# Kernel tuning notes

Hardware: AMD Instinct MI355X
Metric: run time of the kernel (lower is better)

The kernel has to match this reference:

```python
import jax, jax.numpy as jnp
import numpy as np

N_NODES = 100000
N_EDGES = 3200000
F_IN = 256
H = 256
L = 256
BN_EPS = 1e-5


def gcn_conv(x, src, dst, deg_inv_sqrt, W, b):
    # x: [N, Fin]; src/dst: [E+N] (self-loops appended); returns [N, Fout]
    h = x @ W  # dense transform first (Fout may be < Fin)
    norm = deg_inv_sqrt[src] * deg_inv_sqrt[dst]  # [E+N]
    msg = h[src] * norm[:, None]                  # gather
    out = jax.ops.segment_sum(msg, dst, num_segments=N_NODES)  # scatter-add
    return out + b


def batch_norm(x, gamma, beta):
    # BatchNorm1d in training mode: per-feature mean/var over the node dim
    mean = jnp.mean(x, axis=0)
    var = jnp.var(x, axis=0)
    return (x - mean) * jax.lax.rsqrt(var + BN_EPS) * gamma + beta


def setup_inputs() -> dict:
    key = jax.random.key(0)
    ks = jax.random.split(key, 8)
    x = jax.random.normal(ks[0], (N_NODES, F_IN), dtype=jnp.float32)
    edge_index = jax.random.randint(ks[1], (2, N_EDGES), 0, N_NODES, dtype=jnp.int64)
    # glorot-ish init for weights
    W1 = jax.random.normal(ks[2], (F_IN, H), dtype=jnp.float32) * (1.0 / np.sqrt(F_IN))
    b1 = jnp.zeros((H,), dtype=jnp.float32)
    W_mu = jax.random.normal(ks[3], (H, L), dtype=jnp.float32) * (1.0 / np.sqrt(H))
    b_mu = jnp.zeros((L,), dtype=jnp.float32)
    W_ls = jax.random.normal(ks[4], (H, L), dtype=jnp.float32) * (1.0 / np.sqrt(H))
    b_ls = jnp.zeros((L,), dtype=jnp.float32)
    gamma = jnp.ones((H,), dtype=jnp.float32)
    beta = jnp.zeros((H,), dtype=jnp.float32)
    return {"x": x, "edge_index": edge_index, "W1": W1, "b1": b1,
            "W_mu": W_mu, "b_mu": b_mu, "W_ls": W_ls, "b_ls": b_ls,
            "gamma": gamma, "beta": beta}


def reference(x, edge_index, W1, b1, W_mu, b_mu, W_ls, b_ls, gamma, beta):
    # Add self-loops once (shared across the three GCNConv layers)
    loop = jnp.arange(N_NODES, dtype=edge_index.dtype)
    src = jnp.concatenate([edge_index[0], loop])
    dst = jnp.concatenate([edge_index[1], loop])
    deg = jax.ops.segment_sum(jnp.ones_like(dst, dtype=jnp.float32), dst,
                              num_segments=N_NODES)
    deg_inv_sqrt = jnp.where(deg > 0, jax.lax.rsqrt(jnp.maximum(deg, 1.0)), 0.0)

    h = gcn_conv(x, src, dst, deg_inv_sqrt, W1, b1)
    h = jax.nn.relu(batch_norm(h, gamma, beta))
    mu = gcn_conv(h, src, dst, deg_inv_sqrt, W_mu, b_mu)
    logstd = gcn_conv(h, src, dst, deg_inv_sqrt, W_ls, b_ls)
    return (mu, logstd)
```

## Files before the change

### kernel.cpp

```cpp
#include <hip/hip_runtime.h>
#include <hip/hip_bf16.h>

#define FEAT 256
#define NPB 512
#define NPB_SHIFT 9
#define MAXBINS 256
#define CAP 20480
#define BIN_CHUNK 8192

typedef __attribute__((ext_vector_type(8))) short bf16x8;
typedef __attribute__((ext_vector_type(8))) ushort u16x8;
typedef __attribute__((ext_vector_type(4))) float f32x4;

__device__ __forceinline__ float bf2f(ushort h) {
    union { unsigned u; float f; } v; v.u = ((unsigned)h) << 16; return v.f;
}
__device__ __forceinline__ ushort f2bf(float f) {
    union { float f; unsigned u; } v; v.f = f;
    unsigned u = v.u;
    return (ushort)((u + 0x7FFFu + ((u >> 16) & 1u)) >> 16);
}


__global__ __launch_bounds__(256) void k_bin(const int* __restrict__ ei, int E, int N,
                                             int* __restrict__ bincur,
                                             int2* __restrict__ binbuf, int nbins) {
    __shared__ int hist[MAXBINS];
    __shared__ int base[MAXBINS];
    int t = threadIdx.x;
    int T = E + N;
    int start = blockIdx.x * BIN_CHUNK;
    int end = min(start + BIN_CHUNK, T);
    for (int b = t; b < nbins; b += 256) hist[b] = 0;
    __syncthreads();
    for (int idx = start + t; idx < end; idx += 256) {
        int d = (idx < E) ? ei[E + idx] : idx - E;
        atomicAdd(&hist[d >> NPB_SHIFT], 1);
    }
    __syncthreads();
    for (int b = t; b < nbins; b += 256) {
        int c = hist[b];
        base[b] = c ? (b * CAP + atomicAdd(&bincur[b], c)) : 0;
        hist[b] = 0;
    }
    __syncthreads();
    for (int idx = start + t; idx < end; idx += 256) {
        int s, d;
        if (idx < E) { s = ei[idx]; d = ei[E + idx]; }
        else         { s = idx - E; d = idx - E; }
        int b = d >> NPB_SHIFT;
        int local = atomicAdd(&hist[b], 1);
        binbuf[base[b] + local] = make_int2(s, d);
    }
}


__global__ __launch_bounds__(512) void k_scanb(const int* __restrict__ bsum,
                                               int* __restrict__ bpre,
                                               int* __restrict__ offs_n, int nb) {
    __shared__ int s[512];
    int t = threadIdx.x;
    int v = (t < nb) ? bsum[t] : 0;
    s[t] = v;
    __syncthreads();
    for (int d = 1; d < 512; d <<= 1) {
        int x = (t >= d) ? s[t - d] : 0;
        __syncthreads();
        s[t] += x;
        __syncthreads();
    }
    if (t < nb) bpre[t] = s[t] - v;
    if (t == nb - 1) offs_n[0] = s[t];
}


__global__ __launch_bounds__(512) void k_histcsr(const int2* __restrict__ binbuf,
                                                 const int* __restrict__ bincur,
                                                 const int* __restrict__ bpre,
                                                 int* __restrict__ offs,
                                                 float* __restrict__ dis,
                                                 int* __restrict__ csr, int N) {
    __shared__ int h[NPB];
    __shared__ int cur[NPB];
    int b = blockIdx.x;
    int t = threadIdx.x;
    int node0 = b * NPB;
    int nn = min(NPB, N - node0);
    h[t] = 0; cur[t] = 0;
    __syncthreads();
    int cnt = bincur[b];
    int base = b * CAP;
    for (int i = t; i < cnt; i += 512) {
        atomicAdd(&h[binbuf[base + i].y - node0], 1);
    }
    __syncthreads();
    int v = h[t];
    for (int d = 1; d < 512; d <<= 1) {
        int x = (t >= d) ? h[t - d] : 0;
        __syncthreads();
        h[t] += x;
        __syncthreads();
    }
    int myoff = bpre[b] + h[t] - v;
    if (t < nn) {
        offs[node0 + t] = myoff;
        dis[node0 + t] = rsqrtf((float)v);
    }
    h[t] = myoff;
    __syncthreads();
    for (int i = t; i < cnt; i += 512) {
        int2 e = binbuf[base + i];
        int ld = e.y - node0;
        int c = atomicAdd(&cur[ld], 1);
        csr[h[ld] + c] = e.x;
    }
}


__global__ __launch_bounds__(256) void k_cvt(const float* __restrict__ x,
                                             ushort* __restrict__ y,
                                             const float* __restrict__ dis, int n4) {
    int i = blockIdx.x * blockDim.x + threadIdx.x;
    int stride = gridDim.x * blockDim.x;
    for (; i < n4; i += stride) {
        float d = dis[i >> 6];
        float4 v = ((const float4*)x)[i];
        ushort4 o;
        o.x = f2bf(v.x * d); o.y = f2bf(v.y * d);
        o.z = f2bf(v.z * d); o.w = f2bf(v.w * d);
        ((ushort4*)y)[i] = o;
    }
}


__global__ void k_wprep(const float* __restrict__ W1, const float* __restrict__ Wmu,
                        const float* __restrict__ Wls, const float* __restrict__ bmu,
                        const float* __restrict__ bls,
                        ushort* __restrict__ Wt1, ushort* __restrict__ Wtc,
                        float* __restrict__ biasc, float* __restrict__ bnacc) {
    int i = blockIdx.x * 256 + threadIdx.x;
    int m = i >> 16;
    int j = i & 65535;
    int n = j >> 8, k = j & 255;
    const float* W = (m == 0) ? W1 : (m == 1) ? Wmu : Wls;
    ushort v = f2bf(W[k * 256 + n]);
    if (m == 0) Wt1[j] = v;
    else if (m == 1) Wtc[j] = v;
    else Wtc[65536 + j] = v;
    if (i < 512) { biasc[i] = (i < 256) ? bmu[i] : bls[i - 256]; bnacc[i] = 0.f; }
}


__global__ __launch_bounds__(256) void k_agg(const ushort* __restrict__ in,
                                             ushort* __restrict__ out,
                                             const int* __restrict__ offs,
                                             const int* __restrict__ csr,
                                             const float* __restrict__ dis, int N) {
    int wid = blockIdx.x * 4 + ((int)threadIdx.x >> 6);
    if (wid >= N) return;
    int lane = threadIdx.x & 63;
    int half = lane >> 5;
    int l32 = lane & 31;
    int beg = offs[wid], end = offs[wid + 1];
    float acc[8] = {};
    int k = beg;
    for (; k + 16 <= end; k += 16) {
        int s0 = csr[k + half];
        int s1 = csr[k + 2 + half];
        int s2 = csr[k + 4 + half];
        int s3 = csr[k + 6 + half];
        int s4 = csr[k + 8 + half];
        int s5 = csr[k + 10 + half];
        int s6 = csr[k + 12 + half];
        int s7 = csr[k + 14 + half];
        bf16x8 v0 = *(const bf16x8*)(in + (size_t)s0 * FEAT + l32 * 8);
        bf16x8 v1 = *(const bf16x8*)(in + (size_t)s1 * FEAT + l32 * 8);
        bf16x8 v2 = *(const bf16x8*)(in + (size_t)s2 * FEAT + l32 * 8);
        bf16x8 v3 = *(const bf16x8*)(in + (size_t)s3 * FEAT + l32 * 8);
        bf16x8 v4 = *(const bf16x8*)(in + (size_t)s4 * FEAT + l32 * 8);
        bf16x8 v5 = *(const bf16x8*)(in + (size_t)s5 * FEAT + l32 * 8);
        bf16x8 v6 = *(const bf16x8*)(in + (size_t)s6 * FEAT + l32 * 8);
        bf16x8 v7 = *(const bf16x8*)(in + (size_t)s7 * FEAT + l32 * 8);
        #pragma unroll
        for (int j = 0; j < 8; ++j) {
            float t0 = bf2f((ushort)v0[j]) + bf2f((ushort)v1[j]);
            float t1 = bf2f((ushort)v2[j]) + bf2f((ushort)v3[j]);
            float t2 = bf2f((ushort)v4[j]) + bf2f((ushort)v5[j]);
            float t3 = bf2f((ushort)v6[j]) + bf2f((ushort)v7[j]);
            acc[j] += (t0 + t1) + (t2 + t3);
        }
    }
    for (; k + 2 <= end; k += 2) {
        int s = csr[k + half];
        bf16x8 v = *(const bf16x8*)(in + (size_t)s * FEAT + l32 * 8);
        #pragma unroll
        for (int j = 0; j < 8; ++j) acc[j] += bf2f((ushort)v[j]);
    }
    if (k < end && half == 0) {
        int s = csr[k];
        bf16x8 v = *(const bf16x8*)(in + (size_t)s * FEAT + l32 * 8);
        #pragma unroll
        for (int j = 0; j < 8; ++j) acc[j] += bf2f((ushort)v[j]);
    }
    #pragma unroll
    for (int j = 0; j < 8; ++j) acc[j] += __shfl_xor(acc[j], 32, 64);
    if (half == 0) {
        float d = dis[wid];
        u16x8 o;
        #pragma unroll
        for (int j = 0; j < 8; ++j) o[j] = f2bf(acc[j] * d);
        *(u16x8*)(out + (size_t)wid * FEAT + l32 * 8) = o;
    }
}


template <bool BF16OUT>
__global__ __launch_bounds__(256) void k_gemm(const ushort* __restrict__ A,
                                              const ushort* __restrict__ Bt,
                                              const float* __restrict__ bias,
                                              float* __restrict__ C0,
                                              float* __restrict__ C1,
                                              ushort* __restrict__ Cb,
                                              float* __restrict__ bnacc,
                                              int M, int split) {
    __shared__ ushort As[128 * 64];
    __shared__ ushort Bs[128 * 64];
    int t = threadIdx.x;
    int lane = t & 63;
    int wave = t >> 6;
    int wrow = wave >> 1, wcol = wave & 1;
    int bx = blockIdx.x, by = blockIdx.y;
    int lo = lane & 15, g = lane >> 4;
    f32x4 acc[4][4] = {};
    int chunk = t & 7;
    int row4 = t >> 3;

    for (int kt = 0; kt < 4; ++kt) {
        int k0 = kt * 64;
        #pragma unroll
        for (int i = 0; i < 4; ++i) {
            int r = row4 + i * 32;
            int lc = chunk ^ (r & 7);
            int gr = by * 128 + r;
            bf16x8 av = {};
            if (gr < M) av = *(const bf16x8*)(A + (size_t)gr * 256 + k0 + lc * 8);
            *(bf16x8*)(As + r * 64 + chunk * 8) = av;
            int gn = bx * 128 + r;
            bf16x8 bv = *(const bf16x8*)(Bt + (size_t)gn * 256 + k0 + lc * 8);
            *(bf16x8*)(Bs + r * 64 + chunk * 8) = bv;
        }
        __syncthreads();
        #pragma unroll
        for (int h = 0; h < 2; ++h) {
            bf16x8 af[4], bfr[4];
            #pragma unroll
            for (int m = 0; m < 4; ++m) {
                int r = wrow * 64 + m * 16 + lo;
                af[m] = *(const bf16x8*)(As + r * 64 + (((h * 4 + g) ^ (r & 7)) * 8));
            }
            #pragma unroll
            for (int n = 0; n < 4; ++n) {
                int r = wcol * 64 + n * 16 + lo;
                bfr[n] = *(const bf16x8*)(Bs + r * 64 + (((h * 4 + g) ^ (r & 7)) * 8));
            }
            #pragma unroll
            for (int m = 0; m < 4; ++m)
                #pragma unroll
                for (int n = 0; n < 4; ++n)
                    acc[m][n] = __builtin_amdgcn_mfma_f32_16x16x32_bf16(
                        af[m], bfr[n], acc[m][n], 0, 0, 0);
        }
        __syncthreads();
    }
    #pragma unroll
    for (int n = 0; n < 4; ++n) {
        int gc = bx * 128 + wcol * 64 + n * 16 + lo;
        float bb = bias[gc];
        float s = 0.f, q = 0.f;
        #pragma unroll
        for (int m = 0; m < 4; ++m) {
            f32x4 v = acc[m][n];
            #pragma unroll
            for (int r = 0; r < 4; ++r) {
                int grow = by * 128 + wrow * 64 + m * 16 + g * 4 + r;
                if (grow < M) {
                    float val = v[r] + bb;
                    if (BF16OUT) {
                        Cb[(size_t)grow * 256 + gc] = f2bf(val);
                        s += val; q += val * val;
                    } else {
                        float* Cp = C0; int cc = gc;
                        if (gc >= split) { Cp = C1; cc = gc - split; }
                        __builtin_nontemporal_store(val, &Cp[(size_t)grow * 256 + cc]);
                    }
                }
            }
        }
        if (BF16OUT) {
            s += __shfl_xor(s, 16, 64); s += __shfl_xor(s, 32, 64);
            q += __shfl_xor(q, 16, 64); q += __shfl_xor(q, 32, 64);
            if (g == 0) {
                atomicAdd(&bnacc[gc], s);
                atomicAdd(&bnacc[256 + gc], q);
            }
        }
    }
}


__global__ __launch_bounds__(256) void k_bnapply(const ushort* __restrict__ h,
                                                 ushort* __restrict__ o,
                                                 const float* __restrict__ acc,
                                                 const float* __restrict__ gamma,
                                                 const float* __restrict__ beta,
                                                 const float* __restrict__ dis, int Nn) {
    int c4 = (threadIdx.x & 63) * 4;
    int rof = (int)threadIdx.x >> 6;
    float inv = 1.0f / (float)Nn;
    float g[4], b[4];
    #pragma unroll
    for (int j = 0; j < 4; ++j) {
        float mean = acc[c4 + j] * inv;
        float var = acc[FEAT + c4 + j] * inv - mean * mean;
        float rs = rsqrtf(var + 1e-5f);
        g[j] = gamma[c4 + j] * rs;
        b[j] = beta[c4 + j] - mean * g[j];
    }
    for (int r = blockIdx.x * 4 + rof; r < Nn; r += gridDim.x * 4) {
        float d = dis[r];
        ushort4 v = *(const ushort4*)(h + (size_t)r * FEAT + c4);
        float o0 = bf2f(v.x) * g[0] + b[0], o1 = bf2f(v.y) * g[1] + b[1];
        float o2 = bf2f(v.z) * g[2] + b[2], o3 = bf2f(v.w) * g[3] + b[3];
        ushort4 ov;
        ov.x = f2bf((o0 > 0.f ? o0 : 0.f) * d);
        ov.y = f2bf((o1 > 0.f ? o1 : 0.f) * d);
        ov.z = f2bf((o2 > 0.f ? o2 : 0.f) * d);
        ov.w = f2bf((o3 > 0.f ? o3 : 0.f) * d);
        *(ushort4*)(o + (size_t)r * FEAT + c4) = ov;
    }
}


extern "C" void kernel_launch(void* const* d_in, const int* in_sizes, int n_in,
                              void* d_out, int out_size, void* d_ws, size_t ws_size,
                              hipStream_t stream) {
    const float* x     = (const float*)d_in[0];
    const int*   ei    = (const int*)d_in[1];
    const float* W1    = (const float*)d_in[2];
    const float* b1    = (const float*)d_in[3];
    const float* Wmu   = (const float*)d_in[4];
    const float* bmu   = (const float*)d_in[5];
    const float* Wls   = (const float*)d_in[6];
    const float* bls   = (const float*)d_in[7];
    const float* gamma = (const float*)d_in[8];
    const float* beta  = (const float*)d_in[9];

    int N = in_sizes[0] / FEAT;
    int E = in_sizes[1] / 2;
    int nbins = (N + NPB - 1) / NPB;
    int T = E + N;

    float* out = (float*)d_out;
    float* mu  = out;
    float* ls  = out + (size_t)N * FEAT;
    ushort* xtab = (ushort*)mu;
    ushort* H1b  = (ushort*)ls;

    char* p = (char*)d_ws;
    auto alloc = [&](size_t bytes) -> void* {
        void* r = (void*)p;
        p += (bytes + 255) & ~(size_t)255;
        return r;
    };
    ushort* Abuf  = (ushort*)alloc((size_t)N * FEAT * 2);
    int2*   binbuf= (int2*)  alloc((size_t)nbins * CAP * 8);
    int*    csr   = (int*)   alloc((size_t)T * 4);
    int*    offs  = (int*)   alloc((size_t)(N + 1) * 4);
    float*  dis   = (float*) alloc((size_t)N * 4);
    float*  bnacc = (float*) alloc(512 * 4);
    ushort* Wt1   = (ushort*)alloc(65536 * 2);
    ushort* Wtc   = (ushort*)alloc(131072 * 2);
    float*  biasc = (float*) alloc(512 * 4);
    int*    bpre  = (int*)   alloc((size_t)nbins * 4);
    int*    bincur= (int*)   alloc((size_t)nbins * 4);

    hipMemsetAsync(bincur, 0, (size_t)nbins * 4, stream);
    k_bin<<<(T + BIN_CHUNK - 1) / BIN_CHUNK, 256, 0, stream>>>(ei, E, N, bincur, binbuf, nbins);

    k_scanb<<<1, 512, 0, stream>>>(bincur, bpre, offs + N, nbins);
    k_histcsr<<<nbins, 512, 0, stream>>>(binbuf, bincur, bpre, offs, dis, csr, N);

    k_wprep<<<768, 256, 0, stream>>>(W1, Wmu, Wls, bmu, bls, Wt1, Wtc, biasc, bnacc);
    k_cvt<<<2048, 256, 0, stream>>>(x, xtab, dis, N * FEAT / 4);

    k_agg<<<(N + 3) / 4, 256, 0, stream>>>(xtab, Abuf, offs, csr, dis, N);

    dim3 g1(FEAT / 128, (N + 127) / 128);
    k_gemm<true><<<g1, 256, 0, stream>>>(Abuf, Wt1, b1, nullptr, nullptr, H1b, bnacc, N, FEAT);

    k_bnapply<<<2048, 256, 0, stream>>>(H1b, xtab, bnacc, gamma, beta, dis, N);

    k_agg<<<(N + 3) / 4, 256, 0, stream>>>(xtab, Abuf, offs, csr, dis, N);

    dim3 g2(512 / 128, (N + 127) / 128);
    k_gemm<false><<<g2, 256, 0, stream>>>(Abuf, Wtc, biasc, mu, ls, nullptr, nullptr, N, FEAT);
}
```

Before: 752.7 us.

## Keep full A row-tile in LDS across all output columns; fold bin scan into histcsr

The GEMM now loads a whole 128x256 A tile into LDS once per block and loops over all output column groups, so A is read from global memory only once instead of once per column block. The launch grid becomes 1D over row blocks. LDS use rises to about 80KB per block, which lowers occupancy, and each block runs the column loops serially. Separately, the single-block bin prefix scan kernel is removed and every histcsr block recomputes the scan in shared memory, saving one launch at the cost of redundant work per block.

```diff
diff --git a/kernel.cpp b/kernel.cpp
--- a/kernel.cpp
+++ b/kernel.cpp
@@ -55,40 +55,30 @@
 }
 
 
-__global__ __launch_bounds__(512) void k_scanb(const int* __restrict__ bsum,
-                                               int* __restrict__ bpre,
-                                               int* __restrict__ offs_n, int nb) {
-    __shared__ int s[512];
-    int t = threadIdx.x;
-    int v = (t < nb) ? bsum[t] : 0;
-    s[t] = v;
-    __syncthreads();
-    for (int d = 1; d < 512; d <<= 1) {
-        int x = (t >= d) ? s[t - d] : 0;
-        __syncthreads();
-        s[t] += x;
-        __syncthreads();
-    }
-    if (t < nb) bpre[t] = s[t] - v;
-    if (t == nb - 1) offs_n[0] = s[t];
-}
-
-
 __global__ __launch_bounds__(512) void k_histcsr(const int2* __restrict__ binbuf,
                                                  const int* __restrict__ bincur,
-                                                 const int* __restrict__ bpre,
                                                  int* __restrict__ offs,
                                                  float* __restrict__ dis,
-                                                 int* __restrict__ csr, int N) {
+                                                 int* __restrict__ csr, int N, int nbins) {
+    __shared__ int bsh[256];
     __shared__ int h[NPB];
     __shared__ int cur[NPB];
     int b = blockIdx.x;
     int t = threadIdx.x;
     int node0 = b * NPB;
     int nn = min(NPB, N - node0);
+    if (t < 256) bsh[t] = (t < nbins) ? bincur[t] : 0;
     h[t] = 0; cur[t] = 0;
     __syncthreads();
+    for (int d = 1; d < 256; d <<= 1) {
+        int x = (t < 256 && t >= d) ? bsh[t - d] : 0;
+        __syncthreads();
+        if (t < 256) bsh[t] += x;
+        __syncthreads();
+    }
     int cnt = bincur[b];
+    int bpre = bsh[b] - cnt;
+    if (b == 0 && t == 0) offs[N] = bsh[nbins - 1];
     int base = b * CAP;
     for (int i = t; i < cnt; i += 512) {
         atomicAdd(&h[binbuf[base + i].y - node0], 1);
@@ -101,7 +91,7 @@
         h[t] += x;
         __syncthreads();
     }
-    int myoff = bpre[b] + h[t] - v;
+    int myoff = bpre + h[t] - v;
     if (t < nn) {
         offs[node0 + t] = myoff;
         dis[node0 + t] = rsqrtf((float)v);
@@ -214,7 +204,7 @@
 }
 
 
-template <bool BF16OUT>
+template <int NCOL, bool BF16OUT>
 __global__ __launch_bounds__(256) void k_gemm(const ushort* __restrict__ A,
                                               const ushort* __restrict__ Bt,
                                               const float* __restrict__ bias,
@@ -223,85 +213,94 @@
                                               ushort* __restrict__ Cb,
                                               float* __restrict__ bnacc,
                                               int M, int split) {
-    __shared__ ushort As[128 * 64];
+    __shared__ ushort At[128 * 256];
     __shared__ ushort Bs[128 * 64];
     int t = threadIdx.x;
     int lane = t & 63;
     int wave = t >> 6;
-    int wrow = wave >> 1, wcol = wave & 1;
-    int bx = blockIdx.x, by = blockIdx.y;
+    int wr = wave >> 1, wc = wave & 1;
+    int by = blockIdx.x;
     int lo = lane & 15, g = lane >> 4;
-    f32x4 acc[4][4] = {};
-    int chunk = t & 7;
-    int row4 = t >> 3;
-
-    for (int kt = 0; kt < 4; ++kt) {
-        int k0 = kt * 64;
+
+    #pragma unroll
+    for (int i = 0; i < 16; ++i) {
+        int idx = t + i * 256;
+        int r = idx >> 5;
+        int c = idx & 31;
+        int gr = by * 128 + r;
+        bf16x8 av = {};
+        if (gr < M) av = *(const bf16x8*)(A + (size_t)gr * 256 + c * 8);
+        int pc = (c & 24) | ((c & 7) ^ (r & 7));
+        *(bf16x8*)(At + r * 256 + pc * 8) = av;
+    }
+    __syncthreads();
+
+    constexpr int NH = NCOL / 128;
+    for (int nh = 0; nh < NH; ++nh) {
+        f32x4 acc[4][4] = {};
+        for (int kt = 0; kt < 4; ++kt) {
+            #pragma unroll
+            for (int u = 0; u < 4; ++u) {
+                int idx = t + u * 256;
+                int r = idx >> 3, c = idx & 7;
+                int lc = c ^ (r & 7);
+                bf16x8 bv = *(const bf16x8*)(Bt + (size_t)(nh * 128 + r) * 256 + kt * 64 + lc * 8);
+                *(bf16x8*)(Bs + r * 64 + c * 8) = bv;
+            }
+            __syncthreads();
+            #pragma unroll
+            for (int h = 0; h < 2; ++h) {
+                bf16x8 af[4], bfr[4];
+                #pragma unroll
+                for (int m = 0; m < 4; ++m) {
+                    int r = wr * 64 + m * 16 + lo;
+                    af[m] = *(const bf16x8*)(At + r * 256 + (kt * 8 + ((h * 4 + g) ^ (r & 7))) * 8);
+                }
+                #pragma unroll
+                for (int n = 0; n < 4; ++n) {
+                    int r = wc * 64 + n * 16 + lo;
+                    bfr[n] = *(const bf16x8*)(Bs + r * 64 + ((h * 4 + g) ^ (r & 7)) * 8);
+                }
+                #pragma unroll
+                for (int m = 0; m < 4; ++m)
+                    #pragma unroll
+                    for (int n = 0; n < 4; ++n)
+                        acc[m][n] = __builtin_amdgcn_mfma_f32_16x16x32_bf16(
+                            af[m], bfr[n], acc[m][n], 0, 0, 0);
+            }
+            __syncthreads();
+        }
         #pragma unroll
-        for (int i = 0; i < 4; ++i) {
-            int r = row4 + i * 32;
-            int lc = chunk ^ (r & 7);
-            int gr = by * 128 + r;
-            bf16x8 av = {};
-            if (gr < M) av = *(const bf16x8*)(A + (size_t)gr * 256 + k0 + lc * 8);
-            *(bf16x8*)(As + r * 64 + chunk * 8) = av;
-            int gn = bx * 128 + r;
-            bf16x8 bv = *(const bf16x8*)(Bt + (size_t)gn * 256 + k0 + lc * 8);
-            *(bf16x8*)(Bs + r * 64 + chunk * 8) = bv;
-        }
-        __syncthreads();
-        #pragma unroll
-        for (int h = 0; h < 2; ++h) {
-            bf16x8 af[4], bfr[4];
+        for (int n = 0; n < 4; ++n) {
+            int gc = nh * 128 + wc * 64 + n * 16 + lo;
+            float bb = bias[gc];
+            float s = 0.f, q = 0.f;
             #pragma unroll
             for (int m = 0; m < 4; ++m) {
-                int r = wrow * 64 + m * 16 + lo;
-                af[m] = *(const bf16x8*)(As + r * 64 + (((h * 4 + g) ^ (r & 7)) * 8));
-            }
-            #pragma unroll
-            for (int n = 0; n < 4; ++n) {
-                int r = wcol * 64 + n * 16 + lo;
-                bfr[n] = *(const bf16x8*)(Bs + r * 64 + (((h * 4 + g) ^ (r & 7)) * 8));
-            }
-            #pragma unroll
-            for (int m = 0; m < 4; ++m)
+                f32x4 v = acc[m][n];
                 #pragma unroll
-                for (int n = 0; n < 4; ++n)
-                    acc[m][n] = __builtin_amdgcn_mfma_f32_16x16x32_bf16(
-                        af[m], bfr[n], acc[m][n], 0, 0, 0);
-        }
-        __syncthreads();
-    }
-    #pragma unroll
-    for (int n = 0; n < 4; ++n) {
-        int gc = bx * 128 + wcol * 64 + n * 16 + lo;
-        float bb = bias[gc];
-        float s = 0.f, q = 0.f;
-        #pragma unroll
-        for (int m = 0; m < 4; ++m) {
-            f32x4 v = acc[m][n];
-            #pragma unroll
-            for (int r = 0; r < 4; ++r) {
-                int grow = by * 128 + wrow * 64 + m * 16 + g * 4 + r;
-                if (grow < M) {
-                    float val = v[r] + bb;
-                    if (BF16OUT) {
-                        Cb[(size_t)grow * 256 + gc] = f2bf(val);
-                        s += val; q += val * val;
-                    } else {
-                        float* Cp = C0; int cc = gc;
-                        if (gc >= split) { Cp = C1; cc = gc - split; }
-                        __builtin_nontemporal_store(val, &Cp[(size_t)grow * 256 + cc]);
+                for (int r4 = 0; r4 < 4; ++r4) {
+                    int grow = by * 128 + wr * 64 + m * 16 + g * 4 + r4;
+                    if (grow < M) {
+                        float val = v[r4] + bb;
+                        if (BF16OUT) {
+                            Cb[(size_t)grow * 256 + gc] = f2bf(val);
+                            s += val; q += val * val;
+                        } else {
+                            float* Cp = C0; int cc = gc;
+                            if (gc >= split) { Cp = C1; cc = gc - split; }
+                            __builtin_nontemporal_store(val, &Cp[(size_t)grow * 256 + cc]);
+                        }
                     }
                 }
             }
-        }
-        if (BF16OUT) {
-            s += __shfl_xor(s, 16, 64); s += __shfl_xor(s, 32, 64);
-            q += __shfl_xor(q, 16, 64); q += __shfl_xor(q, 32, 64);
-            if (g == 0) {
-                atomicAdd(&bnacc[gc], s);
-                atomicAdd(&bnacc[256 + gc], q);
+            if (BF16OUT) {
+                s += __shfl_xor(s, 16, 64); s += __shfl_xor(s, 32, 64);
+                q += __shfl_xor(q, 16, 64); q += __shfl_xor(q, 32, 64);
+                if (g == 0) {
+                    atomicAdd(&bnacc[gc], s);
+                    atomicAdd(&bnacc[256 + gc], q);
+                }
             }
         }
     }
@@ -381,27 +380,25 @@
     ushort* Wt1   = (ushort*)alloc(65536 * 2);
     ushort* Wtc   = (ushort*)alloc(131072 * 2);
     float*  biasc = (float*) alloc(512 * 4);
-    int*    bpre  = (int*)   alloc((size_t)nbins * 4);
     int*    bincur= (int*)   alloc((size_t)nbins * 4);
 
     hipMemsetAsync(bincur, 0, (size_t)nbins * 4, stream);
     k_bin<<<(T + BIN_CHUNK - 1) / BIN_CHUNK, 256, 0, stream>>>(ei, E, N, bincur, binbuf, nbins);
 
-    k_scanb<<<1, 512, 0, stream>>>(bincur, bpre, offs + N, nbins);
-    k_histcsr<<<nbins, 512, 0, stream>>>(binbuf, bincur, bpre, offs, dis, csr, N);
+    k_histcsr<<<nbins, 512, 0, stream>>>(binbuf, bincur, offs, dis, csr, N, nbins);
 
     k_wprep<<<768, 256, 0, stream>>>(W1, Wmu, Wls, bmu, bls, Wt1, Wtc, biasc, bnacc);
     k_cvt<<<2048, 256, 0, stream>>>(x, xtab, dis, N * FEAT / 4);
 
+    int gblocks = (N + 127) / 128;
+
     k_agg<<<(N + 3) / 4, 256, 0, stream>>>(xtab, Abuf, offs, csr, dis, N);
 
-    dim3 g1(FEAT / 128, (N + 127) / 128);
-    k_gemm<true><<<g1, 256, 0, stream>>>(Abuf, Wt1, b1, nullptr, nullptr, H1b, bnacc, N, FEAT);
+    k_gemm<256, true><<<gblocks, 256, 0, stream>>>(Abuf, Wt1, b1, nullptr, nullptr, H1b, bnacc, N, 256);
 
     k_bnapply<<<2048, 256, 0, stream>>>(H1b, xtab, bnacc, gamma, beta, dis, N);
 
     k_agg<<<(N + 3) / 4, 256, 0, stream>>>(xtab, Abuf, offs, csr, dis, N);
 
-    dim3 g2(512 / 128, (N + 127) / 128);
-    k_gemm<false><<<g2, 256, 0, stream>>>(Abuf, Wtc, biasc, mu, ls, nullptr, nullptr, N, FEAT);
-}
+    k_gemm<512, false><<<gblocks, 256, 0, stream>>>(Abuf, Wtc, biasc, mu, ls, nullptr, nullptr, N, 256);
+}
```

Result: slower. 773.9 us (+2.8%).
